# Performance work log

Hardware: AMD Instinct MI355X
Metric: run time of the kernel (lower is better)

The kernel has to match this reference:

```python
import jax, jax.numpy as jnp
import numpy as np

B = 32768
BACKCAST = 512
FORECAST = 96
UNITS = 512
THETAS = 32
NG = THETAS // 4  # gaussians
L = BACKCAST + FORECAST


def setup_inputs() -> dict:
    key = jax.random.key(0)
    ks = jax.random.split(key, 8)
    s = 0.02
    inp = {
        'x': jax.random.normal(ks[0], (B, BACKCAST), dtype=jnp.float32),
        'fc_w0': jax.random.normal(ks[1], (UNITS, BACKCAST), dtype=jnp.float32) * s,
        'fc_b0': jnp.zeros((UNITS,), jnp.float32),
        'fc_w1': jax.random.normal(ks[2], (UNITS, UNITS), dtype=jnp.float32) * s,
        'fc_b1': jnp.zeros((UNITS,), jnp.float32),
        'fc_w2': jax.random.normal(ks[3], (UNITS, UNITS), dtype=jnp.float32) * s,
        'fc_b2': jnp.zeros((UNITS,), jnp.float32),
        'fc_w3': jax.random.normal(ks[4], (UNITS, UNITS), dtype=jnp.float32) * s,
        'fc_b3': jnp.zeros((UNITS,), jnp.float32),
        'theta_w': jax.random.normal(ks[5], (THETAS, UNITS), dtype=jnp.float32) * s,
        'fn_g': jnp.ones((NG,), jnp.float32), 'fn_b': jnp.zeros((NG,), jnp.float32),
        'wn_g': jnp.ones((NG,), jnp.float32), 'wn_b': jnp.zeros((NG,), jnp.float32),
    }
    # fixed sinusoidal basis buffers
    freqs = (1.0 / np.arange(2.0, L * 2 + 1, dtype=np.float32))  # [2L-1]
    t_b = np.arange(BACKCAST, dtype=np.float32)
    t_f = np.arange(BACKCAST, BACKCAST + FORECAST, dtype=np.float32)
    arg_b = 2.0 * np.pi * freqs[:, None] * t_b
    arg_f = 2.0 * np.pi * freqs[:, None] * t_f
    inp['freqs'] = jnp.asarray(freqs)
    inp['s_backcast'] = jnp.asarray(np.concatenate([np.sin(arg_b), np.cos(arg_b)], 0))
    inp['s_forecast'] = jnp.asarray(np.concatenate([np.sin(arg_f), np.cos(arg_f)], 0))
    return inp


def _layernorm(v, g, b, eps=1e-5):
    m = jnp.mean(v, axis=-1, keepdims=True)
    var = jnp.mean(jnp.square(v - m), axis=-1, keepdims=True)
    return (v - m) * jax.lax.rsqrt(var + eps) * g + b


def _softplus10(v):
    # torch Softplus(beta=10)
    return jax.nn.softplus(10.0 * v) / 10.0


def reference(x, fc_w0, fc_b0, fc_w1, fc_b1, fc_w2, fc_b2, fc_w3, fc_b3,
              theta_w, fn_g, fn_b, wn_g, wn_b, freqs, s_backcast, s_forecast):
    # fc stack (dropout = identity in eval)
    h = jax.nn.relu(x @ fc_w0.T + fc_b0)
    h = jax.nn.relu(h @ fc_w1.T + fc_b1)
    h = jax.nn.relu(h @ fc_w2.T + fc_b2)
    h = jax.nn.relu(h @ fc_w3.T + fc_b3)
    coeff = h @ theta_w.T  # [B, THETAS]
    p = coeff.reshape(coeff.shape[0], -1, 4)  # [B, NG, 4]
    total_len = s_backcast.shape[1] + s_forecast.shape[1]
    cf = 1.0 / (1.0 + jax.nn.sigmoid(_layernorm(p[..., 3], fn_g, fn_b))[..., None] * total_len)  # [B,NG,1]
    inv_w = cf / jnp.maximum(_softplus10(_layernorm(p[..., 2], wn_g, wn_b))[..., None], 1e-6)
    exponent = jnp.square((freqs - cf) * inv_w) * 0.5  # [B, NG, F]
    norm_amp = jax.nn.softmax(exponent, axis=-1)
    amp_sin = jnp.sum(norm_amp * p[..., 0][..., None], axis=1)  # [B, F]
    amp_cos = jnp.sum(norm_amp * p[..., 1][..., None], axis=1)
    amps = jnp.concatenate([amp_sin, amp_cos], axis=-1)  # [B, 2F]
    backcast = amps @ s_backcast
    forecast = amps @ s_forecast
    return (backcast, forecast)
```

## Files before the change

### kernel.cpp

```cpp
#include <hip/hip_runtime.h>
#include <hip/hip_bf16.h>
#include <math.h>

#define BATCH 32768
#define UNITS 512
#define NF 1215
#define KF 2432
#define NOUT 608

typedef __bf16 bf16x8 __attribute__((ext_vector_type(8)));
typedef float f32x4 __attribute__((ext_vector_type(4)));
typedef short s16x4 __attribute__((ext_vector_type(4)));
typedef short s16x8 __attribute__((ext_vector_type(8)));

__device__ __forceinline__ unsigned short f2b(float f) {
  unsigned u = __builtin_bit_cast(unsigned, f);
  u += 0x7fffu + ((u >> 16) & 1u);
  return (unsigned short)(u >> 16);
}
__device__ __forceinline__ float b2f(unsigned short h) {
  unsigned u = ((unsigned)h) << 16;
  return __builtin_bit_cast(float, u);
}

#if __has_builtin(__builtin_amdgcn_exp2f)
__device__ __forceinline__ float fexp2(float x) { return __builtin_amdgcn_exp2f(x); }
#else
__device__ __forceinline__ float fexp2(float x) { return exp2f(x); }
#endif
#if __has_builtin(__builtin_amdgcn_logf)
__device__ __forceinline__ float flog2(float x) { return __builtin_amdgcn_logf(x); }
#else
__device__ __forceinline__ float flog2(float x) { return log2f(x); }
#endif
#if __has_builtin(__builtin_amdgcn_rcpf)
__device__ __forceinline__ float frcp(float x) { return __builtin_amdgcn_rcpf(x); }
#else
__device__ __forceinline__ float frcp(float x) { return 1.f / x; }
#endif

__device__ __forceinline__ void gload16(const unsigned short* g, unsigned short* l) {
  __builtin_amdgcn_global_load_lds(
      (const __attribute__((address_space(1))) void*)g,
      (__attribute__((address_space(3))) void*)l, 16, 0, 0);
}

__global__ __launch_bounds__(256) void split_k4(
    const float* __restrict__ src, unsigned short* __restrict__ hi,
    unsigned short* __restrict__ lo, int n4)
{
  int i = blockIdx.x * 256 + threadIdx.x;
  int stride = gridDim.x * 256;
  for (; i < n4; i += stride) {
    f32x4 v = ((const f32x4*)src)[i];
    s16x4 h, l;
#pragma unroll
    for (int j = 0; j < 4; ++j) {
      unsigned short hb = f2b(v[j]);
      h[j] = (short)hb;
      l[j] = (short)f2b(v[j] - b2f(hb));
    }
    ((s16x4*)hi)[i] = h;
    ((s16x4*)lo)[i] = l;
  }
}

__global__ __launch_bounds__(256) void st_prep(
    const float* __restrict__ sb, const float* __restrict__ sf,
    unsigned short* __restrict__ st)
{
  __shared__ float tile[32][33];
  int k0 = blockIdx.x * 32, n0 = blockIdx.y * 32;
  int tx = threadIdx.x, ty = threadIdx.y;
#pragma unroll
  for (int yy = 0; yy < 32; yy += 8) {
    int k = k0 + ty + yy, n = n0 + tx;
    float v = 0.f;
    if (k < 2430) {
      if (n < 512) v = sb[(size_t)k * 512 + n];
      else if (n < NOUT) v = sf[(size_t)k * 96 + (n - 512)];
    }
    tile[ty + yy][tx] = v;
  }
  __syncthreads();
#pragma unroll
  for (int yy = 0; yy < 32; yy += 8) {
    int n = n0 + ty + yy, k = k0 + tx;
    st[(size_t)n * KF + k] = f2b(tile[tx][ty + yy]);
  }
}

template <int MODE, int NBN>
__global__ __launch_bounds__(256) void gemm_kernel(
    const unsigned short* __restrict__ Agh, const unsigned short* __restrict__ Agl,
    const unsigned short* __restrict__ Bgh, const unsigned short* __restrict__ Bgl,
    const float* __restrict__ bias,
    unsigned short* __restrict__ Chi, unsigned short* __restrict__ Clo,
    float* __restrict__ outF, int K, int ldA, int ldB)
{
  constexpr bool SPLIT = (MODE == 0);
  __shared__ unsigned short Ah[2][128 * 32];
  __shared__ unsigned short Bh[2][128 * 32];
  __shared__ unsigned short Al[SPLIT ? 2 : 1][SPLIT ? 128 * 32 : 8];
  __shared__ unsigned short Bl[SPLIT ? 2 : 1][SPLIT ? 128 * 32 : 8];

  const int t = threadIdx.x;
  const int lane = t & 63;
  const int w = t >> 6;
  const int wr = w >> 1, wc = w & 1;

  const int lin = blockIdx.x;
  const int xcd = lin & 7;
  const int sub = lin >> 3;
  const long bm = (long)(xcd * 32 + sub / NBN) * 128;
  const int bn = (sub % NBN) * 128;

  const int lr = lane & 15, kg = lane >> 4;

  const int Rw = lane >> 2;
  const int pch = lane & 3;
  const int R1 = w * 16 + Rw;
  const int R2 = (w + 4) * 16 + Rw;
  const int s1 = (pch - (R1 >> 1)) & 3;
  const int s2 = (pch - (R2 >> 1)) & 3;
  const size_t oA1 = (size_t)(bm + R1) * ldA + s1 * 8;
  const size_t oA2 = (size_t)(bm + R2) * ldA + s2 * 8;
  const size_t oB1 = (size_t)(bn + R1) * ldB + s1 * 8;
  const size_t oB2 = (size_t)(bn + R2) * ldB + s2 * 8;

  auto STAGE = [&](int buf, int kt) {
    gload16(Agh + oA1 + kt, &Ah[buf][w * 512]);
    gload16(Agh + oA2 + kt, &Ah[buf][(w + 4) * 512]);
    gload16(Bgh + oB1 + kt, &Bh[buf][w * 512]);
    gload16(Bgh + oB2 + kt, &Bh[buf][(w + 4) * 512]);
    if constexpr (SPLIT) {
      gload16(Agl + oA1 + kt, &Al[buf][w * 512]);
      gload16(Agl + oA2 + kt, &Al[buf][(w + 4) * 512]);
      gload16(Bgl + oB1 + kt, &Bl[buf][w * 512]);
      gload16(Bgl + oB2 + kt, &Bl[buf][(w + 4) * 512]);
    }
  };

  const f32x4 fzero = {0.f, 0.f, 0.f, 0.f};
  f32x4 acc[4][4];
#pragma unroll
  for (int m = 0; m < 4; ++m)
#pragma unroll
    for (int n = 0; n < 4; ++n) acc[m][n] = fzero;

  STAGE(0, 0);
  __syncthreads();

  int cur = 0;
  for (int kt = 0; kt < K; kt += 32) {
    if (kt + 32 < K) STAGE(cur ^ 1, kt + 32);

    bf16x8 bhf[4], blf[4];
#pragma unroll
    for (int n = 0; n < 4; ++n) {
      int R = wc * 64 + n * 16 + lr;
      int phys = R * 32 + (((kg + (R >> 1)) & 3) << 3);
      bhf[n] = *(const bf16x8*)&Bh[cur][phys];
      if constexpr (SPLIT) blf[n] = *(const bf16x8*)&Bl[cur][phys];
    }
#pragma unroll
    for (int m = 0; m < 4; ++m) {
      int R = wr * 64 + m * 16 + lr;
      int phys = R * 32 + (((kg + (R >> 1)) & 3) << 3);
      bf16x8 ahf = *(const bf16x8*)&Ah[cur][phys];
      bf16x8 alf = ahf;
      if constexpr (SPLIT) alf = *(const bf16x8*)&Al[cur][phys];
#pragma unroll
      for (int n = 0; n < 4; ++n) {
        acc[m][n] = __builtin_amdgcn_mfma_f32_16x16x32_bf16(ahf, bhf[n], acc[m][n], 0, 0, 0);
        if constexpr (SPLIT) {
          acc[m][n] = __builtin_amdgcn_mfma_f32_16x16x32_bf16(ahf, blf[n], acc[m][n], 0, 0, 0);
          acc[m][n] = __builtin_amdgcn_mfma_f32_16x16x32_bf16(alf, bhf[n], acc[m][n], 0, 0, 0);
        }
      }
    }
    __syncthreads();
    cur ^= 1;
  }

#pragma unroll
  for (int m = 0; m < 4; ++m) {
#pragma unroll
    for (int n = 0; n < 4; ++n) {
      long gr0 = bm + wr * 64 + m * 16 + kg * 4;
      int gc = bn + wc * 64 + n * 16 + lr;
      if constexpr (MODE == 0) {
        float bv = bias[gc];
#pragma unroll
        for (int r = 0; r < 4; ++r) {
          float o = fmaxf(acc[m][n][r] + bv, 0.f);
          unsigned short h = f2b(o);
          size_t off = (size_t)(gr0 + r) * UNITS + gc;
          Chi[off] = h;
          Clo[off] = f2b(o - b2f(h));
        }
      } else {
        if (gc < NOUT) {
#pragma unroll
          for (int r = 0; r < 4; ++r) {
            float o = acc[m][n][r];
            long row = gr0 + r;
            if (gc < 512) outF[row * 512 + gc] = o;
            else outF[(size_t)BATCH * 512 + row * 96 + (gc - 512)] = o;
          }
        }
      }
    }
  }
}

__global__ __launch_bounds__(256) void coeff_gemm(
    const unsigned short* __restrict__ Agh, const unsigned short* __restrict__ Agl,
    const unsigned short* __restrict__ Bgh, const unsigned short* __restrict__ Bgl,
    float* __restrict__ coeff)
{
  __shared__ unsigned short Ah[128 * 32];
  __shared__ unsigned short Al[128 * 32];
  __shared__ unsigned short Bh[32 * 32];
  __shared__ unsigned short Bl[32 * 32];

  const int t = threadIdx.x;
  const int lane = t & 63;
  const int w = t >> 6;
  const long bm = (long)blockIdx.x * 128;
  const int lr = lane & 15, kg = lane >> 4;

  const f32x4 fzero = {0.f, 0.f, 0.f, 0.f};
  f32x4 acc[2][2];
#pragma unroll
  for (int m = 0; m < 2; ++m)
#pragma unroll
    for (int n = 0; n < 2; ++n) acc[m][n] = fzero;

  for (int kt = 0; kt < 512; kt += 32) {
    __syncthreads();
#pragma unroll
    for (int p = 0; p < 2; ++p) {
      int c = t + 256 * p;
      int row = c >> 2, slot = c & 3;
      int phys = row * 32 + (((slot + (row >> 1)) & 3) << 3);
      size_t go = (size_t)(bm + row) * UNITS + kt + slot * 8;
      *(s16x8*)&Ah[phys] = *(const s16x8*)&Agh[go];
      *(s16x8*)&Al[phys] = *(const s16x8*)&Agl[go];
    }
    if (t < 128) {
      int row = t >> 2, slot = t & 3;
      int phys = row * 32 + (((slot + (row >> 1)) & 3) << 3);
      size_t go = (size_t)row * UNITS + kt + slot * 8;
      *(s16x8*)&Bh[phys] = *(const s16x8*)&Bgh[go];
      *(s16x8*)&Bl[phys] = *(const s16x8*)&Bgl[go];
    }
    __syncthreads();

    bf16x8 bh[2], bl[2];
#pragma unroll
    for (int n = 0; n < 2; ++n) {
      int R = n * 16 + lr;
      int phys = R * 32 + (((kg + (R >> 1)) & 3) << 3);
      bh[n] = *(const bf16x8*)&Bh[phys];
      bl[n] = *(const bf16x8*)&Bl[phys];
    }
#pragma unroll
    for (int m = 0; m < 2; ++m) {
      int R = w * 32 + m * 16 + lr;
      int phys = R * 32 + (((kg + (R >> 1)) & 3) << 3);
      bf16x8 ah = *(const bf16x8*)&Ah[phys];
      bf16x8 al = *(const bf16x8*)&Al[phys];
#pragma unroll
      for (int n = 0; n < 2; ++n) {
        acc[m][n] = __builtin_amdgcn_mfma_f32_16x16x32_bf16(ah, bh[n], acc[m][n], 0, 0, 0);
        acc[m][n] = __builtin_amdgcn_mfma_f32_16x16x32_bf16(ah, bl[n], acc[m][n], 0, 0, 0);
        acc[m][n] = __builtin_amdgcn_mfma_f32_16x16x32_bf16(al, bh[n], acc[m][n], 0, 0, 0);
      }
    }
  }
#pragma unroll
  for (int m = 0; m < 2; ++m)
#pragma unroll
    for (int n = 0; n < 2; ++n) {
      long gr0 = bm + w * 32 + m * 16 + kg * 4;
      int gc = n * 16 + lr;
#pragma unroll
      for (int r = 0; r < 4; ++r)
        coeff[(size_t)(gr0 + r) * 32 + gc] = acc[m][n][r];
    }
}

__global__ __launch_bounds__(256) void gauss_kernel(
    const float* __restrict__ coeff, const float* __restrict__ fn_g,
    const float* __restrict__ fn_b, const float* __restrict__ wn_g,
    const float* __restrict__ wn_b, const float* __restrict__ freqs,
    unsigned short* __restrict__ amps)
{
  const int wid = threadIdx.x >> 6;
  const int t = threadIdx.x & 63;
  const int b = blockIdx.x * 4 + wid;
  const float cv = coeff[(size_t)b * 32 + (t & 31)];
  const float L2E = 1.4426950408889634f;

  float c2[8], c3[8];
  float m2 = 0.f, m3 = 0.f;
#pragma unroll
  for (int g = 0; g < 8; ++g) {
    c2[g] = __shfl(cv, 4 * g + 2);
    c3[g] = __shfl(cv, 4 * g + 3);
    m2 += c2[g]; m3 += c3[g];
  }
  m2 *= 0.125f; m3 *= 0.125f;
  float v2 = 0.f, v3 = 0.f;
#pragma unroll
  for (int g = 0; g < 8; ++g) {
    float d2 = c2[g] - m2; v2 += d2 * d2;
    float d3 = c3[g] - m3; v3 += d3 * d3;
  }
  v2 *= 0.125f; v3 *= 0.125f;
  const float r2 = rsqrtf(v2 + 1e-5f), r3 = rsqrtf(v3 + 1e-5f);

  const float S2 = 0.8493218f;
  const float fv0 = freqs[0], fvL = freqs[NF - 1];
  float aa[8], oo[8], mxm[8];
#pragma unroll
  for (int g = 0; g < 8; ++g) {
    float z3 = (c3[g] - m3) * r3 * fn_g[g] + fn_b[g];
    float sig = frcp(1.f + fexp2(-z3 * L2E));
    float cfg = frcp(1.f + sig * 608.f);
    float z2 = (c2[g] - m2) * r2 * wn_g[g] + wn_b[g];
    float x = 10.f * z2;
    float enx = fexp2(-fabsf(x) * L2E);
    float sp = (fmaxf(x, 0.f) + 0.6931471805599453f * flog2(1.f + enx)) * 0.1f;
    float iwg = cfg * frcp(fmaxf(sp, 1e-6f));
    aa[g] = iwg * S2;
    oo[g] = cfg * iwg * S2;
    float d0 = fmaf(fv0, aa[g], -oo[g]);
    float dL = fmaf(fvL, aa[g], -oo[g]);
    mxm[g] = fmaxf(d0 * d0, dL * dL);
  }

  float sm[8];
#pragma unroll
  for (int g = 0; g < 8; ++g) sm[g] = 0.f;

#pragma unroll
  for (int i = 0; i < 19; ++i) {
    int f = t + 64 * i;
    float fv = freqs[min(f, NF - 1)];
#pragma unroll
    for (int g = 0; g < 8; ++g) {
      float d = fmaf(fv, aa[g], -oo[g]);
      float e = fexp2(fmaf(d, d, -mxm[g]));
      if (i == 18) e = (t == 63) ? 0.f : e;
      sm[g] += e;
    }
  }
  float wsn[8], wcn[8];
#pragma unroll
  for (int g = 0; g < 8; ++g) {
#pragma unroll
    for (int m = 32; m >= 1; m >>= 1) sm[g] += __shfl_xor(sm[g], m);
    float inv = frcp(sm[g]);
    wsn[g] = __shfl(cv, 4 * g + 0) * inv;
    wcn[g] = __shfl(cv, 4 * g + 1) * inv;
  }

  size_t base = (size_t)b * KF;
#pragma unroll
  for (int i = 0; i < 19; ++i) {
    int f = t + 64 * i;
    float fv = freqs[min(f, NF - 1)];
    float as = 0.f, ac = 0.f;
#pragma unroll
    for (int g = 0; g < 8; ++g) {
      float d = fmaf(fv, aa[g], -oo[g]);
      float e = fexp2(fmaf(d, d, -mxm[g]));
      as = fmaf(e, wsn[g], as);
      ac = fmaf(e, wcn[g], ac);
    }
    if (f < NF) {
      amps[base + f] = f2b(as);
      amps[base + NF + f] = f2b(ac);
    }
  }
  if (t == 0) {
    amps[base + 2430] = 0;
    amps[base + 2431] = 0;
  }
}

extern "C" void kernel_launch(void* const* d_in, const int* in_sizes, int n_in,
                              void* d_out, int out_size, void* d_ws, size_t ws_size,
                              hipStream_t stream) {
  (void)in_sizes; (void)n_in; (void)out_size; (void)ws_size;
  const float* x = (const float*)d_in[0];
  const float* fcw[4] = {(const float*)d_in[1], (const float*)d_in[3],
                         (const float*)d_in[5], (const float*)d_in[7]};
  const float* fcb[4] = {(const float*)d_in[2], (const float*)d_in[4],
                         (const float*)d_in[6], (const float*)d_in[8]};
  const float* theta_w = (const float*)d_in[9];
  const float* fn_g = (const float*)d_in[10];
  const float* fn_b = (const float*)d_in[11];
  const float* wn_g = (const float*)d_in[12];
  const float* wn_b = (const float*)d_in[13];
  const float* freqs = (const float*)d_in[14];
  const float* sb = (const float*)d_in[15];
  const float* sf = (const float*)d_in[16];
  float* out = (float*)d_out;

  char* p = (char*)d_ws;
  auto take = [&](size_t bytes) {
    char* r = p;
    p += (bytes + 255) & ~(size_t)255;
    return r;
  };
  unsigned short* h0h = (unsigned short*)take((size_t)BATCH * UNITS * 2);
  unsigned short* h0l = (unsigned short*)take((size_t)BATCH * UNITS * 2);
  unsigned short* h1h = (unsigned short*)take((size_t)BATCH * UNITS * 2);
  unsigned short* h1l = (unsigned short*)take((size_t)BATCH * UNITS * 2);
  unsigned short *wh[4], *wl[4];
  for (int l = 0; l < 4; ++l) {
    wh[l] = (unsigned short*)take((size_t)UNITS * UNITS * 2);
    wl[l] = (unsigned short*)take((size_t)UNITS * UNITS * 2);
  }
  unsigned short* twh = (unsigned short*)take((size_t)32 * UNITS * 2);
  unsigned short* twl = (unsigned short*)take((size_t)32 * UNITS * 2);
  float* coeff = (float*)take((size_t)BATCH * 32 * 4);
  unsigned short* st = (unsigned short*)take((size_t)640 * KF * 2);
  unsigned short* amps = (unsigned short*)take((size_t)BATCH * KF * 2);

  split_k4<<<2048, 256, 0, stream>>>(x, h0h, h0l, BATCH * UNITS / 4);
  for (int l = 0; l < 4; ++l)
    split_k4<<<256, 256, 0, stream>>>(fcw[l], wh[l], wl[l], UNITS * UNITS / 4);
  split_k4<<<16, 256, 0, stream>>>(theta_w, twh, twl, 32 * UNITS / 4);
  st_prep<<<dim3(KF / 32, 640 / 32), dim3(32, 8), 0, stream>>>(sb, sf, st);

  gemm_kernel<0, 4><<<4 * (BATCH / 128), 256, 0, stream>>>(
      h0h, h0l, wh[0], wl[0], fcb[0], h1h, h1l, nullptr, 512, 512, 512);
  gemm_kernel<0, 4><<<4 * (BATCH / 128), 256, 0, stream>>>(
      h1h, h1l, wh[1], wl[1], fcb[1], h0h, h0l, nullptr, 512, 512, 512);
  gemm_kernel<0, 4><<<4 * (BATCH / 128), 256, 0, stream>>>(
      h0h, h0l, wh[2], wl[2], fcb[2], h1h, h1l, nullptr, 512, 512, 512);
  gemm_kernel<0, 4><<<4 * (BATCH / 128), 256, 0, stream>>>(
      h1h, h1l, wh[3], wl[3], fcb[3], h0h, h0l, nullptr, 512, 512, 512);

  coeff_gemm<<<BATCH / 128, 256, 0, stream>>>(h0h, h0l, twh, twl, coeff);

  gauss_kernel<<<BATCH / 4, 256, 0, stream>>>(coeff, fn_g, fn_b, wn_g, wn_b, freqs, amps);

  gemm_kernel<1, 5><<<5 * (BATCH / 128), 256, 0, stream>>>(
      amps, nullptr, st, nullptr, nullptr, nullptr, nullptr, out, KF, KF, KF);
}
```

Baseline: 556.2 us.

## Deepen GEMM LDS prefetch pipeline with vmcnt-based waits and raw barriers

```diff
diff --git a/kernel.cpp b/kernel.cpp
--- a/kernel.cpp
+++ b/kernel.cpp
@@ -45,6 +45,20 @@
       (__attribute__((address_space(3))) void*)l, 16, 0, 0);
 }
 
+__device__ __forceinline__ void wait_vmcnt(int n) {
+  switch (n) {
+    case 0:  asm volatile("s_waitcnt vmcnt(0)" ::: "memory"); break;
+    case 4:  asm volatile("s_waitcnt vmcnt(4)" ::: "memory"); break;
+    case 8:  asm volatile("s_waitcnt vmcnt(8)" ::: "memory"); break;
+    default: asm volatile("s_waitcnt vmcnt(12)" ::: "memory"); break;
+  }
+}
+__device__ __forceinline__ void barrier_raw() {
+  asm volatile("" ::: "memory");
+  __builtin_amdgcn_s_barrier();
+  asm volatile("" ::: "memory");
+}
+
 __global__ __launch_bounds__(256) void split_k4(
     const float* __restrict__ src, unsigned short* __restrict__ hi,
     unsigned short* __restrict__ lo, int n4)
@@ -90,19 +104,22 @@
   }
 }
 
-template <int MODE, int NBN>
+template <int MODE, int NBN, int KTOT>
 __global__ __launch_bounds__(256) void gemm_kernel(
     const unsigned short* __restrict__ Agh, const unsigned short* __restrict__ Agl,
     const unsigned short* __restrict__ Bgh, const unsigned short* __restrict__ Bgl,
     const float* __restrict__ bias,
     unsigned short* __restrict__ Chi, unsigned short* __restrict__ Clo,
-    float* __restrict__ outF, int K, int ldA, int ldB)
+    float* __restrict__ outF, int ldA, int ldB)
 {
   constexpr bool SPLIT = (MODE == 0);
-  __shared__ unsigned short Ah[2][128 * 32];
-  __shared__ unsigned short Bh[2][128 * 32];
-  __shared__ unsigned short Al[SPLIT ? 2 : 1][SPLIT ? 128 * 32 : 8];
-  __shared__ unsigned short Bl[SPLIT ? 2 : 1][SPLIT ? 128 * 32 : 8];
+  constexpr int NBUF = SPLIT ? 2 : 4;
+  constexpr int LPS = SPLIT ? 8 : 4;
+  constexpr int NT = KTOT / 32;
+  __shared__ unsigned short Ah[NBUF][128 * 32];
+  __shared__ unsigned short Bh[NBUF][128 * 32];
+  __shared__ unsigned short Al[SPLIT ? NBUF : 1][SPLIT ? 128 * 32 : 8];
+  __shared__ unsigned short Bl[SPLIT ? NBUF : 1][SPLIT ? 128 * 32 : 8];
 
   const int t = threadIdx.x;
   const int lane = t & 63;
@@ -148,13 +165,17 @@
 #pragma unroll
     for (int n = 0; n < 4; ++n) acc[m][n] = fzero;
 
-  STAGE(0, 0);
-  __syncthreads();
-
-  int cur = 0;
-  for (int kt = 0; kt < K; kt += 32) {
-    if (kt + 32 < K) STAGE(cur ^ 1, kt + 32);
-
+#pragma unroll
+  for (int s = 0; s < NBUF - 1; ++s) STAGE(s, s * 32);
+
+  for (int it = 0; it < NT; ++it) {
+    const int pf = it + NBUF - 1;
+    if (pf < NT) STAGE(pf % NBUF, pf * 32);
+    const int inflight = (NT - it < NBUF ? NT - it : NBUF) - 1;
+    wait_vmcnt(inflight * LPS);
+    barrier_raw();
+
+    const int cur = it % NBUF;
     bf16x8 bhf[4], blf[4];
 #pragma unroll
     for (int n = 0; n < 4; ++n) {
@@ -179,8 +200,7 @@
         }
       }
     }
-    __syncthreads();
-    cur ^= 1;
+    barrier_raw();
   }
 
 #pragma unroll
@@ -437,19 +457,19 @@
   split_k4<<<16, 256, 0, stream>>>(theta_w, twh, twl, 32 * UNITS / 4);
   st_prep<<<dim3(KF / 32, 640 / 32), dim3(32, 8), 0, stream>>>(sb, sf, st);
 
-  gemm_kernel<0, 4><<<4 * (BATCH / 128), 256, 0, stream>>>(
-      h0h, h0l, wh[0], wl[0], fcb[0], h1h, h1l, nullptr, 512, 512, 512);
-  gemm_kernel<0, 4><<<4 * (BATCH / 128), 256, 0, stream>>>(
-      h1h, h1l, wh[1], wl[1], fcb[1], h0h, h0l, nullptr, 512, 512, 512);
-  gemm_kernel<0, 4><<<4 * (BATCH / 128), 256, 0, stream>>>(
-      h0h, h0l, wh[2], wl[2], fcb[2], h1h, h1l, nullptr, 512, 512, 512);
-  gemm_kernel<0, 4><<<4 * (BATCH / 128), 256, 0, stream>>>(
-      h1h, h1l, wh[3], wl[3], fcb[3], h0h, h0l, nullptr, 512, 512, 512);
+  gemm_kernel<0, 4, 512><<<4 * (BATCH / 128), 256, 0, stream>>>(
+      h0h, h0l, wh[0], wl[0], fcb[0], h1h, h1l, nullptr, 512, 512);
+  gemm_kernel<0, 4, 512><<<4 * (BATCH / 128), 256, 0, stream>>>(
+      h1h, h1l, wh[1], wl[1], fcb[1], h0h, h0l, nullptr, 512, 512);
+  gemm_kernel<0, 4, 512><<<4 * (BATCH / 128), 256, 0, stream>>>(
+      h0h, h0l, wh[2], wl[2], fcb[2], h1h, h1l, nullptr, 512, 512);
+  gemm_kernel<0, 4, 512><<<4 * (BATCH / 128), 256, 0, stream>>>(
+      h1h, h1l, wh[3], wl[3], fcb[3], h0h, h0l, nullptr, 512, 512);
 
   coeff_gemm<<<BATCH / 128, 256, 0, stream>>>(h0h, h0l, twh, twl, coeff);
 
   gauss_kernel<<<BATCH / 4, 256, 0, stream>>>(coeff, fn_g, fn_b, wn_g, wn_b, freqs, amps);
 
-  gemm_kernel<1, 5><<<5 * (BATCH / 128), 256, 0, stream>>>(
-      amps, nullptr, st, nullptr, nullptr, nullptr, nullptr, out, KF, KF, KF);
-}
+  gemm_kernel<1, 5, KF><<<5 * (BATCH / 128), 256, 0, stream>>>(
+      amps, nullptr, st, nullptr, nullptr, nullptr, nullptr, out, KF, KF);
+}
```

Result: slower. 578.7 us (+4.1%).

## Split GEMM kernel; widen final basis GEMM tile and use vmcnt-based pipelining

Applied to the files above, without the earlier changes.

```diff
diff --git a/kernel.cpp b/kernel.cpp
--- a/kernel.cpp
+++ b/kernel.cpp
@@ -45,6 +45,17 @@
       (__attribute__((address_space(3))) void*)l, 16, 0, 0);
 }
 
+template <int N> __device__ __forceinline__ void wait_vm() {
+  if constexpr (N == 0)      asm volatile("s_waitcnt vmcnt(0)" ::: "memory");
+  else if constexpr (N == 7) asm volatile("s_waitcnt vmcnt(7)" ::: "memory");
+  else                       asm volatile("s_waitcnt vmcnt(8)" ::: "memory");
+}
+__device__ __forceinline__ void barrier_raw() {
+  asm volatile("" ::: "memory");
+  __builtin_amdgcn_s_barrier();
+  asm volatile("" ::: "memory");
+}
+
 __global__ __launch_bounds__(256) void split_k4(
     const float* __restrict__ src, unsigned short* __restrict__ hi,
     unsigned short* __restrict__ lo, int n4)
@@ -90,19 +101,18 @@
   }
 }
 
-template <int MODE, int NBN>
-__global__ __launch_bounds__(256) void gemm_kernel(
+template <int NBN>
+__global__ __launch_bounds__(256) void gemm_fc(
     const unsigned short* __restrict__ Agh, const unsigned short* __restrict__ Agl,
     const unsigned short* __restrict__ Bgh, const unsigned short* __restrict__ Bgl,
     const float* __restrict__ bias,
-    unsigned short* __restrict__ Chi, unsigned short* __restrict__ Clo,
-    float* __restrict__ outF, int K, int ldA, int ldB)
+    unsigned short* __restrict__ Chi, unsigned short* __restrict__ Clo)
 {
-  constexpr bool SPLIT = (MODE == 0);
+  constexpr int NT = 512 / 32;
   __shared__ unsigned short Ah[2][128 * 32];
   __shared__ unsigned short Bh[2][128 * 32];
-  __shared__ unsigned short Al[SPLIT ? 2 : 1][SPLIT ? 128 * 32 : 8];
-  __shared__ unsigned short Bl[SPLIT ? 2 : 1][SPLIT ? 128 * 32 : 8];
+  __shared__ unsigned short Al[2][128 * 32];
+  __shared__ unsigned short Bl[2][128 * 32];
 
   const int t = threadIdx.x;
   const int lane = t & 63;
@@ -123,22 +133,20 @@
   const int R2 = (w + 4) * 16 + Rw;
   const int s1 = (pch - (R1 >> 1)) & 3;
   const int s2 = (pch - (R2 >> 1)) & 3;
-  const size_t oA1 = (size_t)(bm + R1) * ldA + s1 * 8;
-  const size_t oA2 = (size_t)(bm + R2) * ldA + s2 * 8;
-  const size_t oB1 = (size_t)(bn + R1) * ldB + s1 * 8;
-  const size_t oB2 = (size_t)(bn + R2) * ldB + s2 * 8;
+  const size_t oA1 = (size_t)(bm + R1) * UNITS + s1 * 8;
+  const size_t oA2 = (size_t)(bm + R2) * UNITS + s2 * 8;
+  const size_t oB1 = (size_t)(bn + R1) * UNITS + s1 * 8;
+  const size_t oB2 = (size_t)(bn + R2) * UNITS + s2 * 8;
 
   auto STAGE = [&](int buf, int kt) {
     gload16(Agh + oA1 + kt, &Ah[buf][w * 512]);
     gload16(Agh + oA2 + kt, &Ah[buf][(w + 4) * 512]);
     gload16(Bgh + oB1 + kt, &Bh[buf][w * 512]);
     gload16(Bgh + oB2 + kt, &Bh[buf][(w + 4) * 512]);
-    if constexpr (SPLIT) {
-      gload16(Agl + oA1 + kt, &Al[buf][w * 512]);
-      gload16(Agl + oA2 + kt, &Al[buf][(w + 4) * 512]);
-      gload16(Bgl + oB1 + kt, &Bl[buf][w * 512]);
-      gload16(Bgl + oB2 + kt, &Bl[buf][(w + 4) * 512]);
-    }
+    gload16(Agl + oA1 + kt, &Al[buf][w * 512]);
+    gload16(Agl + oA2 + kt, &Al[buf][(w + 4) * 512]);
+    gload16(Bgl + oB1 + kt, &Bl[buf][w * 512]);
+    gload16(Bgl + oB2 + kt, &Bl[buf][(w + 4) * 512]);
   };
 
   const f32x4 fzero = {0.f, 0.f, 0.f, 0.f};
@@ -149,11 +157,11 @@
     for (int n = 0; n < 4; ++n) acc[m][n] = fzero;
 
   STAGE(0, 0);
-  __syncthreads();
-
   int cur = 0;
-  for (int kt = 0; kt < K; kt += 32) {
-    if (kt + 32 < K) STAGE(cur ^ 1, kt + 32);
+  for (int it = 0; it < NT; ++it) {
+    if (it + 1 < NT) { STAGE(cur ^ 1, (it + 1) * 32); wait_vm<8>(); }
+    else wait_vm<0>();
+    barrier_raw();
 
     bf16x8 bhf[4], blf[4];
 #pragma unroll
@@ -161,25 +169,22 @@
       int R = wc * 64 + n * 16 + lr;
       int phys = R * 32 + (((kg + (R >> 1)) & 3) << 3);
       bhf[n] = *(const bf16x8*)&Bh[cur][phys];
-      if constexpr (SPLIT) blf[n] = *(const bf16x8*)&Bl[cur][phys];
+      blf[n] = *(const bf16x8*)&Bl[cur][phys];
     }
 #pragma unroll
     for (int m = 0; m < 4; ++m) {
       int R = wr * 64 + m * 16 + lr;
       int phys = R * 32 + (((kg + (R >> 1)) & 3) << 3);
       bf16x8 ahf = *(const bf16x8*)&Ah[cur][phys];
-      bf16x8 alf = ahf;
-      if constexpr (SPLIT) alf = *(const bf16x8*)&Al[cur][phys];
+      bf16x8 alf = *(const bf16x8*)&Al[cur][phys];
 #pragma unroll
       for (int n = 0; n < 4; ++n) {
         acc[m][n] = __builtin_amdgcn_mfma_f32_16x16x32_bf16(ahf, bhf[n], acc[m][n], 0, 0, 0);
-        if constexpr (SPLIT) {
-          acc[m][n] = __builtin_amdgcn_mfma_f32_16x16x32_bf16(ahf, blf[n], acc[m][n], 0, 0, 0);
-          acc[m][n] = __builtin_amdgcn_mfma_f32_16x16x32_bf16(alf, bhf[n], acc[m][n], 0, 0, 0);
-        }
+        acc[m][n] = __builtin_amdgcn_mfma_f32_16x16x32_bf16(ahf, blf[n], acc[m][n], 0, 0, 0);
+        acc[m][n] = __builtin_amdgcn_mfma_f32_16x16x32_bf16(alf, bhf[n], acc[m][n], 0, 0, 0);
       }
     }
-    __syncthreads();
+    barrier_raw();
     cur ^= 1;
   }
 
@@ -189,25 +194,107 @@
     for (int n = 0; n < 4; ++n) {
       long gr0 = bm + wr * 64 + m * 16 + kg * 4;
       int gc = bn + wc * 64 + n * 16 + lr;
-      if constexpr (MODE == 0) {
-        float bv = bias[gc];
+      float bv = bias[gc];
+#pragma unroll
+      for (int r = 0; r < 4; ++r) {
+        float o = fmaxf(acc[m][n][r] + bv, 0.f);
+        unsigned short h = f2b(o);
+        size_t off = (size_t)(gr0 + r) * UNITS + gc;
+        Chi[off] = h;
+        Clo[off] = f2b(o - b2f(h));
+      }
+    }
+  }
+}
+
+__global__ __launch_bounds__(256) void gemm_wide(
+    const unsigned short* __restrict__ Ag, const unsigned short* __restrict__ Bg,
+    float* __restrict__ outF)
+{
+  constexpr int NT = KF / 32;
+  __shared__ unsigned short Ah[2][128 * 32];
+  __shared__ unsigned short Bh[2][320 * 32];
+
+  const int t = threadIdx.x;
+  const int lane = t & 63;
+  const int w = t >> 6;
+  const int wr = w >> 1, wc = w & 1;
+
+  const int lin = blockIdx.x;
+  const int xcd = lin & 7;
+  const int sub = lin >> 3;
+  const long bm = (long)(xcd * 32 + (sub >> 1)) * 128;
+  const int bn = (sub & 1) * 320;
+
+  const int lr = lane & 15, kg = lane >> 4;
+  const int Rl = lane >> 2, pch = lane & 3;
+
+  const int RA1 = w * 16 + Rl, RA2 = (w + 4) * 16 + Rl;
+  const int sA1 = (pch - (RA1 >> 1)) & 3, sA2 = (pch - (RA2 >> 1)) & 3;
+  const size_t oA1 = (size_t)(bm + RA1) * KF + sA1 * 8;
+  const size_t oA2 = (size_t)(bm + RA2) * KF + sA2 * 8;
+  size_t oB[5];
+#pragma unroll
+  for (int j = 0; j < 5; ++j) {
+    int q = w * 5 + j;
+    int R = q * 16 + Rl;
+    int s = (pch - (R >> 1)) & 3;
+    oB[j] = (size_t)(bn + R) * KF + s * 8;
+  }
+
+  auto STAGE = [&](int buf, int kt) {
+    gload16(Ag + oA1 + kt, &Ah[buf][w * 512]);
+    gload16(Ag + oA2 + kt, &Ah[buf][(w + 4) * 512]);
+#pragma unroll
+    for (int j = 0; j < 5; ++j)
+      gload16(Bg + oB[j] + kt, &Bh[buf][(w * 5 + j) * 512]);
+  };
+
+  const f32x4 fzero = {0.f, 0.f, 0.f, 0.f};
+  f32x4 acc[4][10];
+#pragma unroll
+  for (int m = 0; m < 4; ++m)
+#pragma unroll
+    for (int n = 0; n < 10; ++n) acc[m][n] = fzero;
+
+  STAGE(0, 0);
+  int cur = 0;
+  for (int it = 0; it < NT; ++it) {
+    if (it + 1 < NT) { STAGE(cur ^ 1, (it + 1) * 32); wait_vm<7>(); }
+    else wait_vm<0>();
+    barrier_raw();
+
+    bf16x8 af[4];
+#pragma unroll
+    for (int m = 0; m < 4; ++m) {
+      int R = wr * 64 + m * 16 + lr;
+      af[m] = *(const bf16x8*)&Ah[cur][R * 32 + (((kg + (R >> 1)) & 3) << 3)];
+    }
+#pragma unroll
+    for (int n = 0; n < 10; ++n) {
+      int R = wc * 160 + n * 16 + lr;
+      bf16x8 bf = *(const bf16x8*)&Bh[cur][R * 32 + (((kg + (R >> 1)) & 3) << 3)];
+#pragma unroll
+      for (int m = 0; m < 4; ++m)
+        acc[m][n] = __builtin_amdgcn_mfma_f32_16x16x32_bf16(af[m], bf, acc[m][n], 0, 0, 0);
+    }
+    barrier_raw();
+    cur ^= 1;
+  }
+
+#pragma unroll
+  for (int m = 0; m < 4; ++m) {
+#pragma unroll
+    for (int n = 0; n < 10; ++n) {
+      long gr0 = bm + wr * 64 + m * 16 + kg * 4;
+      int gc = bn + wc * 160 + n * 16 + lr;
+      if (gc < NOUT) {
 #pragma unroll
         for (int r = 0; r < 4; ++r) {
-          float o = fmaxf(acc[m][n][r] + bv, 0.f);
-          unsigned short h = f2b(o);
-          size_t off = (size_t)(gr0 + r) * UNITS + gc;
-          Chi[off] = h;
-          Clo[off] = f2b(o - b2f(h));
-        }
-      } else {
-        if (gc < NOUT) {
-#pragma unroll
-          for (int r = 0; r < 4; ++r) {
-            float o = acc[m][n][r];
-            long row = gr0 + r;
-            if (gc < 512) outF[row * 512 + gc] = o;
-            else outF[(size_t)BATCH * 512 + row * 96 + (gc - 512)] = o;
-          }
+          float o = acc[m][n][r];
+          long row = gr0 + r;
+          if (gc < 512) outF[row * 512 + gc] = o;
+          else outF[(size_t)BATCH * 512 + row * 96 + (gc - 512)] = o;
         }
       }
     }
@@ -437,19 +524,18 @@
   split_k4<<<16, 256, 0, stream>>>(theta_w, twh, twl, 32 * UNITS / 4);
   st_prep<<<dim3(KF / 32, 640 / 32), dim3(32, 8), 0, stream>>>(sb, sf, st);
 
-  gemm_kernel<0, 4><<<4 * (BATCH / 128), 256, 0, stream>>>(
-      h0h, h0l, wh[0], wl[0], fcb[0], h1h, h1l, nullptr, 512, 512, 512);
-  gemm_kernel<0, 4><<<4 * (BATCH / 128), 256, 0, stream>>>(
-      h1h, h1l, wh[1], wl[1], fcb[1], h0h, h0l, nullptr, 512, 512, 512);
-  gemm_kernel<0, 4><<<4 * (BATCH / 128), 256, 0, stream>>>(
-      h0h, h0l, wh[2], wl[2], fcb[2], h1h, h1l, nullptr, 512, 512, 512);
-  gemm_kernel<0, 4><<<4 * (BATCH / 128), 256, 0, stream>>>(
-      h1h, h1l, wh[3], wl[3], fcb[3], h0h, h0l, nullptr, 512, 512, 512);
+  gemm_fc<4><<<4 * (BATCH / 128), 256, 0, stream>>>(
+      h0h, h0l, wh[0], wl[0], fcb[0], h1h, h1l);
+  gemm_fc<4><<<4 * (BATCH / 128), 256, 0, stream>>>(
+      h1h, h1l, wh[1], wl[1], fcb[1], h0h, h0l);
+  gemm_fc<4><<<4 * (BATCH / 128), 256, 0, stream>>>(
+      h0h, h0l, wh[2], wl[2], fcb[2], h1h, h1l);
+  gemm_fc<4><<<4 * (BATCH / 128), 256, 0, stream>>>(
+      h1h, h1l, wh[3], wl[3], fcb[3], h0h, h0l);
 
   coeff_gemm<<<BATCH / 128, 256, 0, stream>>>(h0h, h0l, twh, twl, coeff);
 
   gauss_kernel<<<BATCH / 4, 256, 0, stream>>>(coeff, fn_g, fn_b, wn_g, wn_b, freqs, amps);
 
-  gemm_kernel<1, 5><<<5 * (BATCH / 128), 256, 0, stream>>>(
-      amps, nullptr, st, nullptr, nullptr, nullptr, nullptr, out, KF, KF, KF);
-}
+  gemm_wide<<<2 * (BATCH / 128), 256, 0, stream>>>(amps, st, out);
+}
```

Result: faster. 521.0 us (-6.3%).
